# Kernel optimization log

Measured on AMD Instinct MI355X. Metric: run time of the kernel, lower is better.

The kernel has to match this reference:

```python
import jax, jax.numpy as jnp
import numpy as np

N_U = 50000
N_V = 50000
E = 640000
D = 128  # u_dim == v_dim == hid_dim (required for shape consistency)


def setup_inputs() -> dict:
    key = jax.random.key(0)
    ks = jax.random.split(key, 12)
    scale = 1.0 / np.sqrt(D)
    return {
        "X_u": jax.random.normal(ks[0], (N_U, D), dtype=jnp.float32),
        "X_v": jax.random.normal(ks[1], (N_V, D), dtype=jnp.float32),
        "edge_u": jax.random.randint(ks[2], (E,), 0, N_U, dtype=jnp.int32),
        "edge_v": jax.random.randint(ks[3], (E,), 0, N_V, dtype=jnp.int32),
        "W0": jax.random.uniform(ks[4], (D, D), jnp.float32, -scale, scale),
        "b0": jax.random.uniform(ks[5], (D,), jnp.float32, -scale, scale),
        "W1": jax.random.uniform(ks[6], (D, D), jnp.float32, -scale, scale),
        "b1": jax.random.uniform(ks[7], (D,), jnp.float32, -scale, scale),
        "W2": jax.random.uniform(ks[8], (D, D), jnp.float32, -scale, scale),
        "b2": jax.random.uniform(ks[9], (D,), jnp.float32, -scale, scale),
    }


def reference(X_u, X_v, edge_u, edge_v, W0, b0, W1, b1, W2, b2):
    # bipartite scatter-sum aggregations over the edge list
    def v2u(X):  # X: [N_V, D] -> [N_U, D]
        return jax.ops.segment_sum(X[edge_v], edge_u, num_segments=N_U)

    def u2v(X):  # X: [N_U, D] -> [N_V, D]
        return jax.ops.segment_sum(X[edge_u], edge_v, num_segments=N_V)

    # layer 0 (even): Linear(v_dim->hid) on X_v, then v2u sum
    last_X_u = v2u(X_v @ W0 + b0)
    # layer 1 (odd): Linear(u_dim->hid) on last_X_u, then u2v sum
    last_X_v = u2v(last_X_u @ W1 + b1)
    # layer 2 (even): Linear(v_dim->hid) on last_X_v, then v2u sum
    last_X_u = v2u(last_X_v @ W2 + b2)
    return last_X_u
```

## Files before the change

### kernel.cpp

```cpp
#include <hip/hip_runtime.h>

#define D 128
#define NROW 50000
#define NEDGE 640000
#define CAP 64

#define RBLK 160
#define EPB  4000
#define NBKT 196
#define CELL 64

typedef __attribute__((ext_vector_type(8))) short short8;
typedef __attribute__((ext_vector_type(4))) float f32x4;

__device__ __forceinline__ unsigned short f2bf(float f) {
    unsigned u = __float_as_uint(f);
    unsigned r = (u + 0x7fff + ((u >> 16) & 1)) >> 16;
    return (unsigned short)r;
}
__device__ __forceinline__ void acc2(float& e, float& o, unsigned g) {
    e += __uint_as_float(g << 16);
    o += __uint_as_float(g & 0xffff0000u);
}

__global__ __launch_bounds__(256) void route_gemm1(const int* __restrict__ eu,
                                                   const int* __restrict__ ev,
                                                   unsigned int* __restrict__ recbuf_u,
                                                   int* __restrict__ counts_u,
                                                   unsigned int* __restrict__ recbuf_v,
                                                   int* __restrict__ counts_v,
                                                   const float* __restrict__ W0,
                                                   const float* __restrict__ b0,
                                                   const float* __restrict__ b1,
                                                   const float* __restrict__ W1,
                                                   float* __restrict__ T) {
    const int blk = blockIdx.x, tid = threadIdx.x;
    if (blk < RBLK) {
        __shared__ int cnt_s[NBKT];
        __shared__ unsigned int rec_s[NBKT * CELL];
        const int base = blk * EPB;
        for (int dir = 0; dir < 2; dir++) {
            const int* __restrict__ kk = dir ? ev : eu;
            const int* __restrict__ pp = dir ? eu : ev;
            unsigned int* __restrict__ recbuf = dir ? recbuf_v : recbuf_u;
            int* __restrict__ counts = dir ? counts_v : counts_u;
            if (tid < NBKT) cnt_s[tid] = 0;
            __syncthreads();
            for (int e0 = tid; e0 < EPB; e0 += 256) {
                int e = base + e0;
                int key = kk[e], pay = pp[e];
                int k = key >> 8;
                int p = atomicAdd(&cnt_s[k], 1);
                if (p < CELL) rec_s[k * CELL + p] = ((unsigned)key << 16) | (unsigned)pay;
            }
            __syncthreads();
            if (tid < NBKT) {
                int c = cnt_s[tid];
                counts[blk * NBKT + tid] = (c < CELL) ? c : CELL;
            }
            const int wave = tid >> 6, lane = tid & 63;
            for (int k = wave; k < NBKT; k += 4) {
                int c = cnt_s[k]; c = (c < CELL) ? c : CELL;
                if (lane < c)
                    recbuf[(size_t)(k * RBLK + blk) * CELL + lane] = rec_s[k * CELL + lane];
            }
            __syncthreads();
        }
    } else {
        __shared__ float R[2][128];
        int idx = blk - RBLK;
        int sub = tid >> 7, j = tid & 127;
        int i = idx * 2 + sub;
        bool valid = (i < 130);
        const float* row = nullptr;
        if (valid && i < 128) row = W0 + i * D;
        else if (valid && i == 128) row = b0;
        R[sub][j] = row ? row[j] : 0.f;
        __syncthreads();
        if (!valid) return;
        if (i == 129) { T[129 * D + j] = b1[j]; return; }
        float acc = 0.f;
#pragma unroll 8
        for (int k = 0; k < 128; k++) acc += R[sub][k] * W1[k * D + j];
        T[i * D + j] = acc;
    }
}

__global__ __launch_bounds__(256) void ellbuild_cvt_sg2(const unsigned int* __restrict__ recbuf_u,
                                                        const int* __restrict__ counts_u,
                                                        const unsigned int* __restrict__ recbuf_v,
                                                        const int* __restrict__ counts_v,
                                                        unsigned short* __restrict__ ell_u,
                                                        int* __restrict__ cnt_u,
                                                        unsigned short* __restrict__ ell_v,
                                                        int* __restrict__ cnt_v,
                                                        const float4* __restrict__ Xv4,
                                                        ushort4* __restrict__ Xb4,
                                                        const float* __restrict__ T,
                                                        const float* __restrict__ W2,
                                                        float* __restrict__ P,
                                                        unsigned short* __restrict__ PbT) {
    const int blk = blockIdx.x, tid = threadIdx.x;
    if (blk < 2 * NBKT) {
        const int dir = (blk >= NBKT) ? 1 : 0;
        const int k = dir ? blk - NBKT : blk;
        const unsigned int* __restrict__ recbuf = dir ? recbuf_v : recbuf_u;
        const int* __restrict__ counts = dir ? counts_v : counts_u;
        unsigned short* __restrict__ ell = dir ? ell_v : ell_u;
        int* __restrict__ cnt = dir ? cnt_v : cnt_u;

        __shared__ __align__(16) unsigned short ell_s[256 * CAP];
        __shared__ int cnt_s[256];
        __shared__ int seg_c[RBLK];
        cnt_s[tid] = 0;
        if (tid < RBLK) seg_c[tid] = counts[tid * NBKT + k];
        __syncthreads();

        const int wave = tid >> 6, lane = tid & 63;
        const unsigned int* rb = recbuf + (size_t)k * RBLK * CELL;
        int b = wave;
        int c0 = seg_c[b];
        unsigned int r0 = 0;
        if (lane < c0) r0 = rb[b * CELL + lane];
        while (b < RBLK) {
            int bn = b + 4;
            int c1 = 0; unsigned int r1 = 0;
            if (bn < RBLK) { c1 = seg_c[bn]; if (lane < c1) r1 = rb[bn * CELL + lane]; }
            if (lane < c0) {
                int lr = (r0 >> 16) & 255;
                int p = atomicAdd(&cnt_s[lr], 1);
                if (p < CAP) ell_s[lr * CAP + p] = (unsigned short)(r0 & 0xffff);
            }
            b = bn; c0 = c1; r0 = r1;
        }
        __syncthreads();
        const int row0 = k << 8;
        const int nrows = (row0 + 256 <= NROW) ? 256 : (NROW - row0);
        const uint4* src = (const uint4*)ell_s;
        uint4* dst = (uint4*)(ell + (size_t)row0 * CAP);
        for (int i = tid; i < nrows * 8; i += 256) dst[i] = src[i];
        if (tid < nrows) cnt[row0 + tid] = cnt_s[tid];
    } else if (blk < 2 * NBKT + 6250) {
        int i = (blk - 2 * NBKT) * 256 + tid;
        float4 v = Xv4[i];
        ushort4 o;
        o.x = f2bf(v.x); o.y = f2bf(v.y); o.z = f2bf(v.z); o.w = f2bf(v.w);
        Xb4[i] = o;
    } else {
        __shared__ float R[2][128];
        int idx = blk - (2 * NBKT + 6250);
        int sub = tid >> 7, j = tid & 127;
        int i = idx * 2 + sub;
        bool valid = (i < 130);
        R[sub][j] = valid ? T[i * D + j] : 0.f;
        __syncthreads();
        if (!valid) return;
        float acc = 0.f;
#pragma unroll 8
        for (int kk = 0; kk < 128; kk++) acc += R[sub][kk] * W2[kk * D + j];
        P[i * D + j] = acc;
        if (i < 128) PbT[j * 128 + i] = f2bf(acc);
    }
}

__device__ __forceinline__ void gather_body(const unsigned short* __restrict__ A,
                                            const int* __restrict__ cnt,
                                            const unsigned short* __restrict__ ell,
                                            unsigned short* __restrict__ OUTb,
                                            int blk) {
    int r = blk * 16 + (threadIdx.x >> 4);
    int c = threadIdx.x & 15;
    int n = cnt[r]; n = (n < CAP) ? n : CAP;
    const unsigned short* idx = ell + (size_t)r * CAP;
    float a0 = 0.f, a1 = 0.f, a2 = 0.f, a3 = 0.f, a4 = 0.f, a5 = 0.f, a6 = 0.f, a7 = 0.f;
    int i = 0;
    for (; i + 4 <= n; i += 4) {
        int s0 = idx[i], s1 = idx[i + 1], s2 = idx[i + 2], s3 = idx[i + 3];
        uint4 q0 = *(const uint4*)(A + (size_t)s0 * D + c * 8);
        uint4 q1 = *(const uint4*)(A + (size_t)s1 * D + c * 8);
        uint4 q2 = *(const uint4*)(A + (size_t)s2 * D + c * 8);
        uint4 q3 = *(const uint4*)(A + (size_t)s3 * D + c * 8);
        acc2(a0, a1, q0.x); acc2(a2, a3, q0.y); acc2(a4, a5, q0.z); acc2(a6, a7, q0.w);
        acc2(a0, a1, q1.x); acc2(a2, a3, q1.y); acc2(a4, a5, q1.z); acc2(a6, a7, q1.w);
        acc2(a0, a1, q2.x); acc2(a2, a3, q2.y); acc2(a4, a5, q2.z); acc2(a6, a7, q2.w);
        acc2(a0, a1, q3.x); acc2(a2, a3, q3.y); acc2(a4, a5, q3.z); acc2(a6, a7, q3.w);
    }
    for (; i < n; i++) {
        uint4 q0 = *(const uint4*)(A + (size_t)idx[i] * D + c * 8);
        acc2(a0, a1, q0.x); acc2(a2, a3, q0.y); acc2(a4, a5, q0.z); acc2(a6, a7, q0.w);
    }
    uint4 o;
    o.x = (unsigned)f2bf(a0) | ((unsigned)f2bf(a1) << 16);
    o.y = (unsigned)f2bf(a2) | ((unsigned)f2bf(a3) << 16);
    o.z = (unsigned)f2bf(a4) | ((unsigned)f2bf(a5) << 16);
    o.w = (unsigned)f2bf(a6) | ((unsigned)f2bf(a7) << 16);
    *(uint4*)(OUTb + (size_t)r * D + c * 8) = o;
}

__global__ __launch_bounds__(256) void gather1_tk(const unsigned short* __restrict__ A,
                                                  const int* __restrict__ cnt_u,
                                                  const unsigned short* __restrict__ ell_u,
                                                  unsigned short* __restrict__ OUTb,
                                                  const int* __restrict__ cnt_v,
                                                  const unsigned short* __restrict__ ell_v,
                                                  int* __restrict__ t) {
    if (blockIdx.x < 3125) {
        gather_body(A, cnt_u, ell_u, OUTb, blockIdx.x);
    } else {
        int v = (blockIdx.x - 3125) * 256 + threadIdx.x;
        if (v >= NROW) return;
        int n = cnt_v[v]; n = (n < CAP) ? n : CAP;
        const unsigned short* row = ell_v + (size_t)v * CAP;
        int s = 0;
        for (int i = 0; i < n; i++) s += cnt_u[row[i]];
        t[v] = s;
    }
}

__global__ __launch_bounds__(256) void gather2_g23(const unsigned short* __restrict__ A,
                                                   const int* __restrict__ cnt_v,
                                                   const unsigned short* __restrict__ ell_v,
                                                   unsigned short* __restrict__ OUTb,
                                                   const int* __restrict__ cnt_u,
                                                   const unsigned short* __restrict__ ell_u,
                                                   const int* __restrict__ t,
                                                   int* __restrict__ g2, int* __restrict__ g3) {
    if (blockIdx.x < 3125) {
        gather_body(A, cnt_v, ell_v, OUTb, blockIdx.x);
    } else {
        int u = (blockIdx.x - 3125) * 256 + threadIdx.x;
        if (u >= NROW) return;
        int n = cnt_u[u]; n = (n < CAP) ? n : CAP;
        const unsigned short* row = ell_u + (size_t)u * CAP;
        int a = 0, b = 0;
        for (int i = 0; i < n; i++) {
            int s = row[i];
            a += t[s];
            b += cnt_v[s];
        }
        g2[u] = a;
        g3[u] = b;
    }
}

__global__ __launch_bounds__(256) void gather_rows(const unsigned short* __restrict__ A,
                                                   const int* __restrict__ cnt,
                                                   const unsigned short* __restrict__ ell,
                                                   unsigned short* __restrict__ OUTb) {
    gather_body(A, cnt, ell, OUTb, blockIdx.x);
}

__global__ __launch_bounds__(256) void gemm_final_mfma(const unsigned short* __restrict__ Z,
                                                       const unsigned short* __restrict__ PbT,
                                                       const float* __restrict__ P,
                                                       const float* __restrict__ b2,
                                                       const int* __restrict__ g2,
                                                       const int* __restrict__ g3,
                                                       const int* __restrict__ du,
                                                       float* __restrict__ OUT) {
    const int wave = threadIdx.x >> 6;
    const int lane = threadIdx.x & 63;
    const int ml = lane & 15;
    const int quad = lane >> 4;
    const int m0 = blockIdx.x * 64 + wave * 16;
    if (m0 >= NROW) return;

    const uint4* zr = (const uint4*)(Z + (size_t)(m0 + ml) * D);

    f32x4 acc[8];
#pragma unroll
    for (int nt = 0; nt < 8; nt++) acc[nt] = (f32x4){0.f, 0.f, 0.f, 0.f};

#pragma unroll
    for (int kc = 0; kc < 4; kc++) {
        short8 a = __builtin_bit_cast(short8, zr[kc * 4 + quad]);
#pragma unroll
        for (int nt = 0; nt < 8; nt++) {
            const uint4* br = (const uint4*)(PbT + (size_t)(nt * 16 + ml) * D);
            short8 b = __builtin_bit_cast(short8, br[kc * 4 + quad]);
            acc[nt] = __builtin_amdgcn_mfma_f32_16x16x32_bf16(a, b, acc[nt], 0, 0, 0);
        }
    }

    float sg2[4], sg3[4], sdu[4];
#pragma unroll
    for (int reg = 0; reg < 4; reg++) {
        int r = m0 + quad * 4 + reg;
        sg2[reg] = (float)g2[r];
        sg3[reg] = (float)g3[r];
        sdu[reg] = (float)du[r];
    }
    const float* c0 = P + 128 * D;
    const float* c1 = P + 129 * D;
#pragma unroll
    for (int nt = 0; nt < 8; nt++) {
        int col = nt * 16 + ml;
        float cc0 = c0[col], cc1 = c1[col], cb2 = b2[col];
#pragma unroll
        for (int reg = 0; reg < 4; reg++) {
            int r = m0 + quad * 4 + reg;
            OUT[(size_t)r * D + col] = acc[nt][reg] + sg2[reg] * cc0 + sg3[reg] * cc1 + sdu[reg] * cb2;
        }
    }
}

extern "C" void kernel_launch(void* const* d_in, const int* in_sizes, int n_in,
                              void* d_out, int out_size, void* d_ws, size_t ws_size,
                              hipStream_t stream) {
    const float* X_v = (const float*)d_in[1];
    const int* edge_u = (const int*)d_in[2];
    const int* edge_v = (const int*)d_in[3];
    const float* W0 = (const float*)d_in[4];
    const float* b0 = (const float*)d_in[5];
    const float* W1 = (const float*)d_in[6];
    const float* b1 = (const float*)d_in[7];
    const float* W2 = (const float*)d_in[8];
    const float* b2 = (const float*)d_in[9];

    char* w = (char*)d_ws;
    unsigned short* A = (unsigned short*)w;
    unsigned short* ell_u = (unsigned short*)(w + 12800000);
    unsigned short* ell_v = ell_u + (size_t)NROW * CAP;
    int* cnt_u = (int*)(ell_v + (size_t)NROW * CAP);
    int* cnt_v = cnt_u + NROW;
    int* tbuf  = cnt_v + NROW;
    int* g2    = tbuf + NROW;
    int* g3    = g2 + NROW;
    float* T   = (float*)(g3 + NROW);
    float* P   = T + 130 * D;
    unsigned short* PbT = (unsigned short*)(P + 130 * D);
    unsigned int* recbuf_u = (unsigned int*)(PbT + 128 * 128);
    unsigned int* recbuf_v = recbuf_u + (size_t)NBKT * RBLK * CELL;
    int* counts_u = (int*)(recbuf_v + (size_t)NBKT * RBLK * CELL);
    int* counts_v = counts_u + NBKT * RBLK;

    float* OUT = (float*)d_out;
    unsigned short* B = (unsigned short*)d_out;

    const dim3 blk(256);

    route_gemm1<<<RBLK + 65, blk, 0, stream>>>(edge_u, edge_v,
                                               recbuf_u, counts_u, recbuf_v, counts_v,
                                               W0, b0, b1, W1, T);
    ellbuild_cvt_sg2<<<2 * NBKT + 6250 + 65, blk, 0, stream>>>(recbuf_u, counts_u,
                                                               recbuf_v, counts_v,
                                                               ell_u, cnt_u, ell_v, cnt_v,
                                                               (const float4*)X_v, (ushort4*)B,
                                                               T, W2, P, PbT);
    gather1_tk<<<3125 + 196, blk, 0, stream>>>(B, cnt_u, ell_u, A, cnt_v, ell_v, tbuf);
    gather2_g23<<<3125 + 196, blk, 0, stream>>>(A, cnt_v, ell_v, B, cnt_u, ell_u, tbuf, g2, g3);
    gather_rows<<<3125, blk, 0, stream>>>(B, cnt_u, ell_u, A);
    gemm_final_mfma<<<782, blk, 0, stream>>>(A, PbT, P, b2, g2, g3, cnt_u, OUT);
}
```

Before: 255.8 us.

## Fuse three gather hops into one cooperative kernel with grid syncs

```diff
diff --git a/kernel.cpp b/kernel.cpp
--- a/kernel.cpp
+++ b/kernel.cpp
@@ -1,4 +1,7 @@
 #include <hip/hip_runtime.h>
+#include <hip/hip_cooperative_groups.h>
+
+namespace cg = cooperative_groups;
 
 #define D 128
 #define NROW 50000
@@ -168,25 +171,46 @@
                                             const unsigned short* __restrict__ ell,
                                             unsigned short* __restrict__ OUTb,
                                             int blk) {
-    int r = blk * 16 + (threadIdx.x >> 4);
-    int c = threadIdx.x & 15;
+    const int r = blk * 16 + (threadIdx.x >> 4);
+    const int c = threadIdx.x & 15;
     int n = cnt[r]; n = (n < CAP) ? n : CAP;
-    const unsigned short* idx = ell + (size_t)r * CAP;
+    const unsigned short* __restrict__ idx = ell + (size_t)r * CAP;
+    const unsigned short* __restrict__ Ac = A + c * 8;
     float a0 = 0.f, a1 = 0.f, a2 = 0.f, a3 = 0.f, a4 = 0.f, a5 = 0.f, a6 = 0.f, a7 = 0.f;
     int i = 0;
-    for (; i + 4 <= n; i += 4) {
-        int s0 = idx[i], s1 = idx[i + 1], s2 = idx[i + 2], s3 = idx[i + 3];
-        uint4 q0 = *(const uint4*)(A + (size_t)s0 * D + c * 8);
-        uint4 q1 = *(const uint4*)(A + (size_t)s1 * D + c * 8);
-        uint4 q2 = *(const uint4*)(A + (size_t)s2 * D + c * 8);
-        uint4 q3 = *(const uint4*)(A + (size_t)s3 * D + c * 8);
+    for (; i + 8 <= n; i += 8) {
+        uint4 iv = *(const uint4*)(idx + i);
+        uint4 q0 = *(const uint4*)(Ac + (size_t)(iv.x & 0xffffu) * D);
+        uint4 q1 = *(const uint4*)(Ac + (size_t)(iv.x >> 16) * D);
+        uint4 q2 = *(const uint4*)(Ac + (size_t)(iv.y & 0xffffu) * D);
+        uint4 q3 = *(const uint4*)(Ac + (size_t)(iv.y >> 16) * D);
+        uint4 q4 = *(const uint4*)(Ac + (size_t)(iv.z & 0xffffu) * D);
+        uint4 q5 = *(const uint4*)(Ac + (size_t)(iv.z >> 16) * D);
+        uint4 q6 = *(const uint4*)(Ac + (size_t)(iv.w & 0xffffu) * D);
+        uint4 q7 = *(const uint4*)(Ac + (size_t)(iv.w >> 16) * D);
         acc2(a0, a1, q0.x); acc2(a2, a3, q0.y); acc2(a4, a5, q0.z); acc2(a6, a7, q0.w);
         acc2(a0, a1, q1.x); acc2(a2, a3, q1.y); acc2(a4, a5, q1.z); acc2(a6, a7, q1.w);
         acc2(a0, a1, q2.x); acc2(a2, a3, q2.y); acc2(a4, a5, q2.z); acc2(a6, a7, q2.w);
         acc2(a0, a1, q3.x); acc2(a2, a3, q3.y); acc2(a4, a5, q3.z); acc2(a6, a7, q3.w);
+        acc2(a0, a1, q4.x); acc2(a2, a3, q4.y); acc2(a4, a5, q4.z); acc2(a6, a7, q4.w);
+        acc2(a0, a1, q5.x); acc2(a2, a3, q5.y); acc2(a4, a5, q5.z); acc2(a6, a7, q5.w);
+        acc2(a0, a1, q6.x); acc2(a2, a3, q6.y); acc2(a4, a5, q6.z); acc2(a6, a7, q6.w);
+        acc2(a0, a1, q7.x); acc2(a2, a3, q7.y); acc2(a4, a5, q7.z); acc2(a6, a7, q7.w);
+    }
+    if (i + 4 <= n) {
+        uint2 iv = *(const uint2*)(idx + i);
+        uint4 q0 = *(const uint4*)(Ac + (size_t)(iv.x & 0xffffu) * D);
+        uint4 q1 = *(const uint4*)(Ac + (size_t)(iv.x >> 16) * D);
+        uint4 q2 = *(const uint4*)(Ac + (size_t)(iv.y & 0xffffu) * D);
+        uint4 q3 = *(const uint4*)(Ac + (size_t)(iv.y >> 16) * D);
+        acc2(a0, a1, q0.x); acc2(a2, a3, q0.y); acc2(a4, a5, q0.z); acc2(a6, a7, q0.w);
+        acc2(a0, a1, q1.x); acc2(a2, a3, q1.y); acc2(a4, a5, q1.z); acc2(a6, a7, q1.w);
+        acc2(a0, a1, q2.x); acc2(a2, a3, q2.y); acc2(a4, a5, q2.z); acc2(a6, a7, q2.w);
+        acc2(a0, a1, q3.x); acc2(a2, a3, q3.y); acc2(a4, a5, q3.z); acc2(a6, a7, q3.w);
+        i += 4;
     }
     for (; i < n; i++) {
-        uint4 q0 = *(const uint4*)(A + (size_t)idx[i] * D + c * 8);
+        uint4 q0 = *(const uint4*)(Ac + (size_t)idx[i] * D);
         acc2(a0, a1, q0.x); acc2(a2, a3, q0.y); acc2(a4, a5, q0.z); acc2(a6, a7, q0.w);
     }
     uint4 o;
@@ -195,6 +219,75 @@
     o.z = (unsigned)f2bf(a4) | ((unsigned)f2bf(a5) << 16);
     o.w = (unsigned)f2bf(a6) | ((unsigned)f2bf(a7) << 16);
     *(uint4*)(OUTb + (size_t)r * D + c * 8) = o;
+}
+
+__device__ __forceinline__ void tk_body(const int* __restrict__ cnt_v,
+                                        const unsigned short* __restrict__ ell_v,
+                                        const int* __restrict__ cnt_u,
+                                        int* __restrict__ t, int v) {
+    if (v >= NROW) return;
+    int n = cnt_v[v]; n = (n < CAP) ? n : CAP;
+    const unsigned short* row = ell_v + (size_t)v * CAP;
+    int s = 0;
+    for (int i = 0; i < n; i += 8) {
+        uint4 iv = *(const uint4*)(row + i);
+        unsigned sx[8] = {iv.x & 0xffffu, iv.x >> 16, iv.y & 0xffffu, iv.y >> 16,
+                          iv.z & 0xffffu, iv.z >> 16, iv.w & 0xffffu, iv.w >> 16};
+#pragma unroll
+        for (int j = 0; j < 8; j++) if (i + j < n) s += cnt_u[sx[j]];
+    }
+    t[v] = s;
+}
+
+__device__ __forceinline__ void g23_body(const int* __restrict__ cnt_u,
+                                         const unsigned short* __restrict__ ell_u,
+                                         const int* __restrict__ cnt_v,
+                                         const int* __restrict__ t,
+                                         int* __restrict__ g2, int* __restrict__ g3, int u) {
+    if (u >= NROW) return;
+    int n = cnt_u[u]; n = (n < CAP) ? n : CAP;
+    const unsigned short* row = ell_u + (size_t)u * CAP;
+    int a = 0, b = 0;
+    for (int i = 0; i < n; i += 8) {
+        uint4 iv = *(const uint4*)(row + i);
+        unsigned sx[8] = {iv.x & 0xffffu, iv.x >> 16, iv.y & 0xffffu, iv.y >> 16,
+                          iv.z & 0xffffu, iv.z >> 16, iv.w & 0xffffu, iv.w >> 16};
+#pragma unroll
+        for (int j = 0; j < 8; j++)
+            if (i + j < n) { a += t[sx[j]]; b += cnt_v[sx[j]]; }
+    }
+    g2[u] = a;
+    g3[u] = b;
+}
+
+__global__ __launch_bounds__(256) void fused_hops(const unsigned short* __restrict__ B,
+                                                  unsigned short* __restrict__ A,
+                                                  const int* __restrict__ cnt_u,
+                                                  const unsigned short* __restrict__ ell_u,
+                                                  const int* __restrict__ cnt_v,
+                                                  const unsigned short* __restrict__ ell_v,
+                                                  int* __restrict__ t,
+                                                  int* __restrict__ g2,
+                                                  int* __restrict__ g3) {
+    cg::grid_group grid = cg::this_grid();
+    unsigned short* Bm = (unsigned short*)B;
+
+    for (int it = blockIdx.x; it < 3125 + 196; it += gridDim.x) {
+        if (it < 3125) gather_body(B, cnt_u, ell_u, A, it);
+        else tk_body(cnt_v, ell_v, cnt_u, t, (it - 3125) * 256 + threadIdx.x);
+    }
+    __threadfence();
+    grid.sync();
+
+    for (int it = blockIdx.x; it < 3125 + 196; it += gridDim.x) {
+        if (it < 3125) gather_body(A, cnt_v, ell_v, Bm, it);
+        else g23_body(cnt_u, ell_u, cnt_v, t, g2, g3, (it - 3125) * 256 + threadIdx.x);
+    }
+    __threadfence();
+    grid.sync();
+
+    for (int it = blockIdx.x; it < 3125; it += gridDim.x)
+        gather_body(Bm, cnt_u, ell_u, A, it);
 }
 
 __global__ __launch_bounds__(256) void gather1_tk(const unsigned short* __restrict__ A,
@@ -204,17 +297,8 @@
                                                   const int* __restrict__ cnt_v,
                                                   const unsigned short* __restrict__ ell_v,
                                                   int* __restrict__ t) {
-    if (blockIdx.x < 3125) {
-        gather_body(A, cnt_u, ell_u, OUTb, blockIdx.x);
-    } else {
-        int v = (blockIdx.x - 3125) * 256 + threadIdx.x;
-        if (v >= NROW) return;
-        int n = cnt_v[v]; n = (n < CAP) ? n : CAP;
-        const unsigned short* row = ell_v + (size_t)v * CAP;
-        int s = 0;
-        for (int i = 0; i < n; i++) s += cnt_u[row[i]];
-        t[v] = s;
-    }
+    if (blockIdx.x < 3125) gather_body(A, cnt_u, ell_u, OUTb, blockIdx.x);
+    else tk_body(cnt_v, ell_v, cnt_u, t, (blockIdx.x - 3125) * 256 + threadIdx.x);
 }
 
 __global__ __launch_bounds__(256) void gather2_g23(const unsigned short* __restrict__ A,
@@ -225,22 +309,8 @@
                                                    const unsigned short* __restrict__ ell_u,
                                                    const int* __restrict__ t,
                                                    int* __restrict__ g2, int* __restrict__ g3) {
-    if (blockIdx.x < 3125) {
-        gather_body(A, cnt_v, ell_v, OUTb, blockIdx.x);
-    } else {
-        int u = (blockIdx.x - 3125) * 256 + threadIdx.x;
-        if (u >= NROW) return;
-        int n = cnt_u[u]; n = (n < CAP) ? n : CAP;
-        const unsigned short* row = ell_u + (size_t)u * CAP;
-        int a = 0, b = 0;
-        for (int i = 0; i < n; i++) {
-            int s = row[i];
-            a += t[s];
-            b += cnt_v[s];
-        }
-        g2[u] = a;
-        g3[u] = b;
-    }
+    if (blockIdx.x < 3125) gather_body(A, cnt_v, ell_v, OUTb, blockIdx.x);
+    else g23_body(cnt_u, ell_u, cnt_v, t, g2, g3, (blockIdx.x - 3125) * 256 + threadIdx.x);
 }
 
 __global__ __launch_bounds__(256) void gather_rows(const unsigned short* __restrict__ A,
@@ -347,8 +417,29 @@
                                                                ell_u, cnt_u, ell_v, cnt_v,
                                                                (const float4*)X_v, (ushort4*)B,
                                                                T, W2, P, PbT);
-    gather1_tk<<<3125 + 196, blk, 0, stream>>>(B, cnt_u, ell_u, A, cnt_v, ell_v, tbuf);
-    gather2_g23<<<3125 + 196, blk, 0, stream>>>(A, cnt_v, ell_v, B, cnt_u, ell_u, tbuf, g2, g3);
-    gather_rows<<<3125, blk, 0, stream>>>(B, cnt_u, ell_u, A);
+
+    {
+        int nb = 0;
+        hipOccupancyMaxActiveBlocksPerMultiprocessor(&nb,
+            reinterpret_cast<const void*>(fused_hops), 256, 0);
+        int dev = 0, ncu = 0;
+        hipGetDevice(&dev);
+        hipDeviceGetAttribute(&ncu, hipDeviceAttributeMultiprocessorCount, dev);
+        if (ncu <= 0) ncu = 256;
+        if (nb <= 0) nb = 4;
+        long long g = (long long)nb * ncu;
+        if (g > 3321) g = 3321;
+        const unsigned short* Bc = B;
+        void* args[] = {(void*)&Bc, (void*)&A, (void*)&cnt_u, (void*)&ell_u,
+                        (void*)&cnt_v, (void*)&ell_v, (void*)&tbuf, (void*)&g2, (void*)&g3};
+        hipError_t e = hipLaunchCooperativeKernel(reinterpret_cast<const void*>(fused_hops),
+                                                  dim3((unsigned)g), blk, args, 0, stream);
+        if (e != hipSuccess) {
+            gather1_tk<<<3125 + 196, blk, 0, stream>>>(B, cnt_u, ell_u, A, cnt_v, ell_v, tbuf);
+            gather2_g23<<<3125 + 196, blk, 0, stream>>>(A, cnt_v, ell_v, B, cnt_u, ell_u, tbuf, g2, g3);
+            gather_rows<<<3125, blk, 0, stream>>>(B, cnt_u, ell_u, A);
+        }
+    }
+
     gemm_final_mfma<<<782, blk, 0, stream>>>(A, PbT, P, b2, g2, g3, cnt_u, OUT);
 }
```

Result: slower. 639.8 us (+150.1%).
